# Kernel optimization log

Measured on AMD Instinct MI355X. Metric: run time of the kernel, lower is better.

Reference implementation:

```python
import jax, jax.numpy as jnp
import numpy as np

N = 10000
E = 160000
D = 512
EPS = 1e-5


def _lin_params(key, out_d, in_d, bias=True):
    k1, k2 = jax.random.split(key)
    s = 1.0 / np.sqrt(in_d)
    W = jax.random.uniform(k1, (out_d, in_d), jnp.float32, -s, s)
    if bias:
        b = jax.random.uniform(k2, (out_d,), jnp.float32, -s, s)
        return W, b
    return (W,)


def setup_inputs() -> dict:
    key = jax.random.key(0)
    ks = jax.random.split(key, 16)
    inp = {
        "x": jax.random.normal(ks[0], (N, D), jnp.float32),
        "edge_index": jax.random.randint(ks[1], (2, E), 0, N, jnp.int64),
    }
    ki = 2
    for l in range(3):
        Wp, bp = _lin_params(ks[ki], D, D); ki += 1
        Wl, bl = _lin_params(ks[ki], D, D); ki += 1
        (Wr,) = _lin_params(ks[ki], D, D, bias=False); ki += 1
        inp[f"Wp{l}"] = Wp; inp[f"bp{l}"] = bp
        inp[f"Wl{l}"] = Wl; inp[f"bl{l}"] = bl
        inp[f"Wr{l}"] = Wr
        if l < 2:  # ReLU+LayerNorm between convs
            inp[f"g{l}"] = jnp.ones((D,), jnp.float32)
            inp[f"be{l}"] = jnp.zeros((D,), jnp.float32)
    return inp


def _sage_conv(x, src, dst, Wp, bp, Wl, bl, Wr):
    # PyG SAGEConv with project=True: project+ReLU messages, mean-aggregate, lin_l + lin_r(root)
    h = jax.nn.relu(x @ Wp.T + bp)                      # [N, D] projected messages
    agg = jax.ops.segment_sum(h[src], dst, num_segments=N)   # gather + scatter-add
    cnt = jax.ops.segment_sum(jnp.ones((src.shape[0],), x.dtype), dst, num_segments=N)
    agg = agg / jnp.maximum(cnt, 1.0)[:, None]          # mean over incoming edges
    return agg @ Wl.T + bl + x @ Wr.T


def _relu_ln(x, g, b):
    x = jax.nn.relu(x)
    mu = jnp.mean(x, axis=-1, keepdims=True)
    var = jnp.mean(jnp.square(x - mu), axis=-1, keepdims=True)
    return (x - mu) * jax.lax.rsqrt(var + EPS) * g + b


def reference(x, edge_index,
              Wp0, bp0, Wl0, bl0, Wr0, g0, be0,
              Wp1, bp1, Wl1, bl1, Wr1, g1, be1,
              Wp2, bp2, Wl2, bl2, Wr2):
    src, dst = edge_index[0], edge_index[1]
    x = _sage_conv(x, src, dst, Wp0, bp0, Wl0, bl0, Wr0)
    x = _relu_ln(x, g0, be0)
    x = _sage_conv(x, src, dst, Wp1, bp1, Wl1, bl1, Wr1)
    x = _relu_ln(x, g1, be1)
    x = _sage_conv(x, src, dst, Wp2, bp2, Wl2, bl2, Wr2)
    return x
```

## Files before the change

### kernel.cpp

```cpp
#include <hip/hip_runtime.h>
#include <cstdint>

#define D 512
#define TM 128
#define TN 64
#define BK 32
#define CAP 64

typedef unsigned short u16;
typedef __bf16 bf16x8 __attribute__((ext_vector_type(8)));
typedef float f32x4 __attribute__((ext_vector_type(4)));

__device__ __forceinline__ float bf2f(u16 u) {
    unsigned int x = ((unsigned int)u) << 16;
    return __builtin_bit_cast(float, x);
}
__device__ __forceinline__ u16 f2bf(float f) {
    unsigned int x = __builtin_bit_cast(unsigned int, f);
    x += 0x7fffu + ((x >> 16) & 1u);
    return (u16)(x >> 16);
}

__device__ __forceinline__ void gload16(const u16* g, u16* l) {
    __builtin_amdgcn_global_load_lds(
        (const __attribute__((address_space(1))) void*)(uintptr_t)g,
        (__attribute__((address_space(3))) void*)(unsigned int)(uintptr_t)l,
        16, 0, 0);
}

__global__ void detect(const u16* __restrict__ xraw, const int* __restrict__ eraw,
                       int* __restrict__ flags)
{
    __shared__ int cf, ci;
    if (threadIdx.x == 0) { cf = 0; ci = 0; }
    __syncthreads();
    int t = threadIdx.x;
    u16 u = xraw[2 * t];
    int e = (u >> 7) & 0xFF;
    if (e >= 110 && e <= 129) atomicAdd(&cf, 1);
    if (eraw[2 * t + 1] == 0) atomicAdd(&ci, 1);
    __syncthreads();
    if (threadIdx.x == 0) {
        flags[0] = (cf >= 128) ? 1 : 0;
        flags[1] = (ci >= 128) ? 1 : 0;
    }
}

__global__ __launch_bounds__(256) void convert_x(
    const void* __restrict__ src, u16* __restrict__ out, const int* __restrict__ flags)
{
    int i = (blockIdx.x * 256 + threadIdx.x) * 8;
    if (flags[0]) {
        *(uint4*)(out + i) = *(const uint4*)((const u16*)src + i);
    } else {
        const float* f = (const float*)src + i;
        float4 a = *(const float4*)f;
        float4 b = *(const float4*)(f + 4);
        u16 r[8] = {f2bf(a.x), f2bf(a.y), f2bf(a.z), f2bf(a.w),
                    f2bf(b.x), f2bf(b.y), f2bf(b.z), f2bf(b.w)};
        *(uint4*)(out + i) = *(uint4*)r;
    }
}

struct Ptrs9  { const void* p[9];  };
struct Ptrs10 { const void* p[10]; };

__global__ __launch_bounds__(256) void convert_mat(
    Ptrs9 s, u16* __restrict__ out, const int* __restrict__ flags)
{
    int m = blockIdx.y;
    const void* src = s.p[m];
    u16* o = out + (size_t)m * D * D;
    int i = (blockIdx.x * 256 + threadIdx.x) * 8;
    if (flags[0]) {
        *(uint4*)(o + i) = *(const uint4*)((const u16*)src + i);
    } else {
        const float* f = (const float*)src + i;
        float4 a = *(const float4*)f;
        float4 b = *(const float4*)(f + 4);
        u16 r[8] = {f2bf(a.x), f2bf(a.y), f2bf(a.z), f2bf(a.w),
                    f2bf(b.x), f2bf(b.y), f2bf(b.z), f2bf(b.w)};
        *(uint4*)(o + i) = *(uint4*)r;
    }
}

__global__ __launch_bounds__(256) void convert_vec(
    Ptrs10 s, float* __restrict__ out, const int* __restrict__ flags)
{
    int b = blockIdx.x;
    const void* src = s.p[b];
#pragma unroll
    for (int j = threadIdx.x * 2; j < threadIdx.x * 2 + 2; j++) {
        float v = flags[0] ? bf2f(((const u16*)src)[j]) : ((const float*)src)[j];
        out[b * 512 + j] = v;
    }
}

__global__ __launch_bounds__(256) void convert_edges(
    const int* __restrict__ eraw, int* __restrict__ esrc, int* __restrict__ edst,
    const int* __restrict__ flags, int E, int Nn)
{
    int e = blockIdx.x * 256 + threadIdx.x;
    if (e >= E) return;
    int s, d;
    if (flags[1]) { s = eraw[2 * e]; d = eraw[2 * (E + e)]; }
    else          { s = eraw[e];     d = eraw[E + e]; }
    esrc[e] = min(max(s, 0), Nn - 1);
    edst[e] = min(max(d, 0), Nn - 1);
}

template <int NPASS, bool RELU, bool FINAL>
__global__ __launch_bounds__(256) void gemm_bt(
    const u16* __restrict__ A0, const u16* __restrict__ B0,
    const u16* __restrict__ A1, const u16* __restrict__ B1,
    const float* __restrict__ bias, void* __restrict__ Cout,
    const int* __restrict__ flags, int M)
{
    __shared__ __align__(16) u16 sA[TM * BK];
    __shared__ __align__(16) u16 sB[TN * BK];

    const int t    = threadIdx.x;
    const int m0   = blockIdx.x * TM;
    const int n0   = blockIdx.y * TN;
    const int wave = t >> 6, lane = t & 63;
    const int wm   = wave >> 1, wn = wave & 1;
    const int lrow = lane & 15, quad = lane >> 4;

    f32x4 acc[4][2];
#pragma unroll
    for (int i = 0; i < 4; i++)
#pragma unroll
        for (int j = 0; j < 2; j++)
#pragma unroll
            for (int r = 0; r < 4; r++) acc[i][j][r] = 0.f;

    const int cA    = (t & 3) * 8;
    const int rowA0 = min(m0 + (t >> 2),      M - 1);
    const int rowA1 = min(m0 + 64 + (t >> 2), M - 1);
    const int rowB  = n0 + (t >> 2);

#pragma unroll 1
    for (int p = 0; p < NPASS; p++) {
        const u16* A = p ? A1 : A0;
        const u16* B = p ? B1 : B0;
        const u16* gA0 = A + (size_t)rowA0 * D + cA;
        const u16* gA1 = A + (size_t)rowA1 * D + cA;
        const u16* gB  = B + (size_t)rowB  * D + cA;

#pragma unroll 1
        for (int k0 = 0; k0 < D; k0 += BK) {
            gload16(gA0 + k0, &sA[(size_t)t * 8]);
            gload16(gA1 + k0, &sA[(size_t)(t + 256) * 8]);
            gload16(gB  + k0, &sB[(size_t)t * 8]);
            __syncthreads();

            bf16x8 af[4], bfr[2];
#pragma unroll
            for (int mi = 0; mi < 4; mi++) {
                int r = wm * 64 + mi * 16 + lrow;
                af[mi] = *(const bf16x8*)&sA[r * BK + quad * 8];
            }
#pragma unroll
            for (int ni = 0; ni < 2; ni++) {
                int r = wn * 32 + ni * 16 + lrow;
                bfr[ni] = *(const bf16x8*)&sB[r * BK + quad * 8];
            }
#pragma unroll
            for (int mi = 0; mi < 4; mi++)
#pragma unroll
                for (int ni = 0; ni < 2; ni++)
                    acc[mi][ni] = __builtin_amdgcn_mfma_f32_16x16x32_bf16(
                        af[mi], bfr[ni], acc[mi][ni], 0, 0, 0);
            __syncthreads();
        }
    }

    const int out_bf16 = FINAL ? flags[0] : 1;
#pragma unroll
    for (int ni = 0; ni < 2; ni++) {
        int col = n0 + wn * 32 + ni * 16 + lrow;
        float bv = bias[col];
#pragma unroll
        for (int mi = 0; mi < 4; mi++) {
            int row0 = m0 + wm * 64 + mi * 16 + quad * 4;
#pragma unroll
            for (int r = 0; r < 4; r++) {
                int row = row0 + r;
                if (row < M) {
                    float v = acc[mi][ni][r] + bv;
                    if (RELU) v = fmaxf(v, 0.f);
                    if (!FINAL || out_bf16)
                        ((u16*)Cout)[(size_t)row * D + col] = f2bf(v);
                    else
                        ((float*)Cout)[(size_t)row * D + col] = v;
                }
            }
        }
    }
}

__global__ void build_bucket(const int* __restrict__ esrc, const int* __restrict__ edst,
                             int* __restrict__ cnt, u16* __restrict__ bucket, int E)
{
    int e = blockIdx.x * 256 + threadIdx.x;
    if (e < E) {
        int d = edst[e];
        int p = atomicAdd(&cnt[d], 1);
        if (p < CAP) bucket[(size_t)d * CAP + p] = (u16)esrc[e];
    }
}

__global__ __launch_bounds__(256) void aggregate(
    const u16* __restrict__ h, const int* __restrict__ cnt,
    const u16* __restrict__ bucket, u16* __restrict__ agg, int M)
{
    const int w = threadIdx.x >> 6, lane = threadIdx.x & 63;
    const int n = blockIdx.x * 4 + w;

    __shared__ u16 sidx[4][CAP];
    int deg = 0, dd = 0;
    if (n < M) {
        deg = cnt[n];
        dd  = min(deg, CAP);
        if (lane < dd) sidx[w][lane] = bucket[(size_t)n * CAP + lane];
    }
    __syncthreads();
    if (n >= M) return;

    float a[8] = {0.f, 0.f, 0.f, 0.f, 0.f, 0.f, 0.f, 0.f};
    int i = 0;
    for (; i + 2 <= dd; i += 2) {
        int s0 = sidx[w][i], s1 = sidx[w][i + 1];
        uint4 v0 = *(const uint4*)(h + (size_t)s0 * D + lane * 8);
        uint4 v1 = *(const uint4*)(h + (size_t)s1 * D + lane * 8);
        const unsigned int* u0 = (const unsigned int*)&v0;
        const unsigned int* u1 = (const unsigned int*)&v1;
#pragma unroll
        for (int j = 0; j < 4; j++) {
            a[2 * j]     += bf2f((u16)(u0[j] & 0xffffu)) + bf2f((u16)(u1[j] & 0xffffu));
            a[2 * j + 1] += bf2f((u16)(u0[j] >> 16))     + bf2f((u16)(u1[j] >> 16));
        }
    }
    if (i < dd) {
        int s0 = sidx[w][i];
        uint4 v0 = *(const uint4*)(h + (size_t)s0 * D + lane * 8);
        const unsigned int* u0 = (const unsigned int*)&v0;
#pragma unroll
        for (int j = 0; j < 4; j++) {
            a[2 * j]     += bf2f((u16)(u0[j] & 0xffffu));
            a[2 * j + 1] += bf2f((u16)(u0[j] >> 16));
        }
    }

    float inv = 1.f / fmaxf((float)deg, 1.f);
    u16 r[8];
#pragma unroll
    for (int j = 0; j < 8; j++) r[j] = f2bf(a[j] * inv);
    *(uint4*)(agg + (size_t)n * D + lane * 8) = *(uint4*)r;
}

__global__ __launch_bounds__(256) void relu_ln(
    const u16* __restrict__ y, const float* __restrict__ g, const float* __restrict__ be,
    u16* __restrict__ out, int M)
{
    const int row  = blockIdx.x * 4 + (threadIdx.x >> 6);
    const int lane = threadIdx.x & 63;
    if (row >= M) return;

    typedef short s16x8 __attribute__((ext_vector_type(8)));
    s16x8 v = *(const s16x8*)(y + (size_t)row * D + lane * 8);
    float f[8], s = 0.f, s2 = 0.f;
#pragma unroll
    for (int i = 0; i < 8; i++) {
        float x = bf2f((u16)v[i]);
        x = fmaxf(x, 0.f);
        f[i] = x; s += x; s2 += x * x;
    }
#pragma unroll
    for (int off = 32; off >= 1; off >>= 1) {
        s  += __shfl_xor(s, off);
        s2 += __shfl_xor(s2, off);
    }
    float mean = s * (1.f / 512.f);
    float var  = s2 * (1.f / 512.f) - mean * mean;
    float rstd = rsqrtf(var + 1e-5f);

    s16x8 res;
#pragma unroll
    for (int i = 0; i < 8; i++) {
        float o = (f[i] - mean) * rstd * g[lane * 8 + i] + be[lane * 8 + i];
        res[i] = (short)f2bf(o);
    }
    *(s16x8*)(out + (size_t)row * D + lane * 8) = res;
}

extern "C" void kernel_launch(void* const* d_in, const int* in_sizes, int n_in,
                              void* d_out, int out_size, void* d_ws, size_t ws_size,
                              hipStream_t stream)
{
    const int M = in_sizes[0] / D;
    const int E = in_sizes[1] / 2;
    const void* xraw = d_in[0];
    const int*  eraw = (const int*)d_in[1];

    const void *Wp[3], *bp[3], *Wl[3], *bl[3], *Wr[3], *g[2], *be[2];
    int idx = 2;
    for (int l = 0; l < 3; l++) {
        Wp[l] = d_in[idx++]; bp[l] = d_in[idx++];
        Wl[l] = d_in[idx++]; bl[l] = d_in[idx++];
        Wr[l] = d_in[idx++];
        if (l < 2) { g[l] = d_in[idx++]; be[l] = d_in[idx++]; }
    }

    char* w = (char*)d_ws;
    auto alloc = [&](size_t bytes) { void* p = w; w += (bytes + 255) & ~(size_t)255; return p; };
    u16*   xb     = (u16*)  alloc((size_t)M * D * 2);
    u16*   h      = (u16*)  alloc((size_t)M * D * 2);
    u16*   agg    = (u16*)  alloc((size_t)M * D * 2);
    u16*   Wb     = (u16*)  alloc((size_t)9 * D * D * 2);
    float* vecf   = (float*)alloc((size_t)10 * 512 * 4);
    int*   esrc   = (int*)  alloc((size_t)E * 4);
    int*   edst   = (int*)  alloc((size_t)E * 4);
    int*   cnt    = (int*)  alloc((size_t)M * 4);
    u16*   bucket = (u16*)  alloc((size_t)M * CAP * 2);
    int*   flags  = (int*)  alloc(256);

    detect<<<1, 256, 0, stream>>>((const u16*)xraw, eraw, flags);

    convert_x<<<dim3(M * D / (256 * 8)), dim3(256), 0, stream>>>(xraw, xb, flags);

    Ptrs9 mats;
    const void* morder[9] = {Wp[0], Wl[0], Wr[0], Wp[1], Wl[1], Wr[1], Wp[2], Wl[2], Wr[2]};
    for (int i = 0; i < 9; i++) mats.p[i] = morder[i];
    convert_mat<<<dim3(D * D / (256 * 8), 9), dim3(256), 0, stream>>>(mats, Wb, flags);

    Ptrs10 vecs;
    const void* vorder[10] = {bp[0], bl[0], g[0], be[0], bp[1], bl[1], g[1], be[1], bp[2], bl[2]};
    for (int i = 0; i < 10; i++) vecs.p[i] = vorder[i];
    convert_vec<<<dim3(10), dim3(256), 0, stream>>>(vecs, vecf, flags);

    convert_edges<<<dim3((E + 255) / 256), dim3(256), 0, stream>>>(eraw, esrc, edst, flags, E, M);

    hipMemsetAsync(cnt, 0, (size_t)M * 4, stream);
    build_bucket<<<dim3((E + 255) / 256), dim3(256), 0, stream>>>(esrc, edst, cnt, bucket, E);

    const u16* WM[9]; for (int i = 0; i < 9; i++) WM[i] = Wb + (size_t)i * D * D;
    const float* VB[10]; for (int i = 0; i < 10; i++) VB[i] = vecf + (size_t)i * 512;

    u16* yb = (u16*)d_out;
    dim3 gg((M + TM - 1) / TM, D / TN);
    const u16* xin = xb;
    for (int l = 0; l < 3; l++) {
        gemm_bt<1, true, false><<<gg, dim3(256), 0, stream>>>(
            xin, WM[l * 3 + 0], xin, WM[l * 3 + 0], VB[l * 4 + 0], h, flags, M);
        aggregate<<<dim3((M + 3) / 4), dim3(256), 0, stream>>>(h, cnt, bucket, agg, M);
        if (l < 2) {
            gemm_bt<2, false, false><<<gg, dim3(256), 0, stream>>>(
                agg, WM[l * 3 + 1], xin, WM[l * 3 + 2], VB[l * 4 + 1], yb, flags, M);
            relu_ln<<<dim3((M + 3) / 4), dim3(256), 0, stream>>>(
                yb, VB[l * 4 + 2], VB[l * 4 + 3], xb, M);
            xin = xb;
        } else {
            gemm_bt<2, false, true><<<gg, dim3(256), 0, stream>>>(
                agg, WM[l * 3 + 1], xin, WM[l * 3 + 2], VB[l * 4 + 1], d_out, flags, M);
        }
    }
}
```

Before: 368.6 us.

## Widen GEMM tile to 128x128, fuse prep kernels, unroll aggregation by four

```diff
diff --git a/kernel.cpp b/kernel.cpp
--- a/kernel.cpp
+++ b/kernel.cpp
@@ -3,7 +3,7 @@
 
 #define D 512
 #define TM 128
-#define TN 64
+#define TN 128
 #define BK 32
 #define CAP 64
 
@@ -28,29 +28,25 @@
         16, 0, 0);
 }
 
-__global__ void detect(const u16* __restrict__ xraw, const int* __restrict__ eraw,
-                       int* __restrict__ flags)
-{
-    __shared__ int cf, ci;
-    if (threadIdx.x == 0) { cf = 0; ci = 0; }
-    __syncthreads();
-    int t = threadIdx.x;
-    u16 u = xraw[2 * t];
+__device__ __forceinline__ bool is_bf16(const u16* xraw) {
+    int lane = threadIdx.x & 63;
+    u16 u = xraw[2 * lane];
     int e = (u >> 7) & 0xFF;
-    if (e >= 110 && e <= 129) atomicAdd(&cf, 1);
-    if (eraw[2 * t + 1] == 0) atomicAdd(&ci, 1);
-    __syncthreads();
-    if (threadIdx.x == 0) {
-        flags[0] = (cf >= 128) ? 1 : 0;
-        flags[1] = (ci >= 128) ? 1 : 0;
-    }
+    unsigned long long b = __ballot(e >= 110 && e <= 129);
+    return __popcll(b) >= 32;
+}
+__device__ __forceinline__ bool is_i64(const int* eraw) {
+    int lane = threadIdx.x & 63;
+    unsigned long long b = __ballot(eraw[2 * lane + 1] == 0);
+    return __popcll(b) >= 32;
 }
 
 __global__ __launch_bounds__(256) void convert_x(
-    const void* __restrict__ src, u16* __restrict__ out, const int* __restrict__ flags)
-{
+    const void* __restrict__ src, u16* __restrict__ out)
+{
+    bool bf = is_bf16((const u16*)src);
     int i = (blockIdx.x * 256 + threadIdx.x) * 8;
-    if (flags[0]) {
+    if (bf) {
         *(uint4*)(out + i) = *(const uint4*)((const u16*)src + i);
     } else {
         const float* f = (const float*)src + i;
@@ -65,48 +61,52 @@
 struct Ptrs9  { const void* p[9];  };
 struct Ptrs10 { const void* p[10]; };
 
-__global__ __launch_bounds__(256) void convert_mat(
-    Ptrs9 s, u16* __restrict__ out, const int* __restrict__ flags)
-{
+__global__ __launch_bounds__(256) void convert_wb(
+    Ptrs9 s, Ptrs10 v, u16* __restrict__ wout, float* __restrict__ vout,
+    const u16* __restrict__ xraw)
+{
+    bool bf = is_bf16(xraw);
     int m = blockIdx.y;
-    const void* src = s.p[m];
-    u16* o = out + (size_t)m * D * D;
-    int i = (blockIdx.x * 256 + threadIdx.x) * 8;
-    if (flags[0]) {
-        *(uint4*)(o + i) = *(const uint4*)((const u16*)src + i);
-    } else {
-        const float* f = (const float*)src + i;
-        float4 a = *(const float4*)f;
-        float4 b = *(const float4*)(f + 4);
-        u16 r[8] = {f2bf(a.x), f2bf(a.y), f2bf(a.z), f2bf(a.w),
-                    f2bf(b.x), f2bf(b.y), f2bf(b.z), f2bf(b.w)};
-        *(uint4*)(o + i) = *(uint4*)r;
-    }
-}
-
-__global__ __launch_bounds__(256) void convert_vec(
-    Ptrs10 s, float* __restrict__ out, const int* __restrict__ flags)
-{
-    int b = blockIdx.x;
-    const void* src = s.p[b];
-#pragma unroll
-    for (int j = threadIdx.x * 2; j < threadIdx.x * 2 + 2; j++) {
-        float v = flags[0] ? bf2f(((const u16*)src)[j]) : ((const float*)src)[j];
-        out[b * 512 + j] = v;
-    }
-}
-
-__global__ __launch_bounds__(256) void convert_edges(
-    const int* __restrict__ eraw, int* __restrict__ esrc, int* __restrict__ edst,
-    const int* __restrict__ flags, int E, int Nn)
-{
+    if (m < 9) {
+        const void* src = s.p[m];
+        u16* o = wout + (size_t)m * D * D;
+        int i = (blockIdx.x * 256 + threadIdx.x) * 8;
+        if (bf) {
+            *(uint4*)(o + i) = *(const uint4*)((const u16*)src + i);
+        } else {
+            const float* f = (const float*)src + i;
+            float4 a = *(const float4*)f;
+            float4 b = *(const float4*)(f + 4);
+            u16 r[8] = {f2bf(a.x), f2bf(a.y), f2bf(a.z), f2bf(a.w),
+                        f2bf(b.x), f2bf(b.y), f2bf(b.z), f2bf(b.w)};
+            *(uint4*)(o + i) = *(uint4*)r;
+        }
+    } else if (blockIdx.x == 0) {
+        for (int b = 0; b < 10; b++) {
+            const void* src = v.p[b];
+            for (int j = threadIdx.x * 2; j < threadIdx.x * 2 + 2; j++) {
+                float val = bf ? bf2f(((const u16*)src)[j]) : ((const float*)src)[j];
+                vout[b * 512 + j] = val;
+            }
+        }
+    }
+}
+
+__global__ void build_bucket(const int* __restrict__ eraw,
+                             int* __restrict__ cnt, u16* __restrict__ bucket,
+                             int E, int Nn)
+{
+    bool i64 = is_i64(eraw);
     int e = blockIdx.x * 256 + threadIdx.x;
-    if (e >= E) return;
-    int s, d;
-    if (flags[1]) { s = eraw[2 * e]; d = eraw[2 * (E + e)]; }
-    else          { s = eraw[e];     d = eraw[E + e]; }
-    esrc[e] = min(max(s, 0), Nn - 1);
-    edst[e] = min(max(d, 0), Nn - 1);
+    if (e < E) {
+        int s, d;
+        if (i64) { s = eraw[2 * e]; d = eraw[2 * (E + e)]; }
+        else     { s = eraw[e];     d = eraw[E + e]; }
+        s = min(max(s, 0), Nn - 1);
+        d = min(max(d, 0), Nn - 1);
+        int p = atomicAdd(&cnt[d], 1);
+        if (p < CAP) bucket[(size_t)d * CAP + p] = (u16)s;
+    }
 }
 
 template <int NPASS, bool RELU, bool FINAL>
@@ -114,7 +114,7 @@
     const u16* __restrict__ A0, const u16* __restrict__ B0,
     const u16* __restrict__ A1, const u16* __restrict__ B1,
     const float* __restrict__ bias, void* __restrict__ Cout,
-    const int* __restrict__ flags, int M)
+    const u16* __restrict__ xraw, int M)
 {
     __shared__ __align__(16) u16 sA[TM * BK];
     __shared__ __align__(16) u16 sB[TN * BK];
@@ -126,59 +126,59 @@
     const int wm   = wave >> 1, wn = wave & 1;
     const int lrow = lane & 15, quad = lane >> 4;
 
-    f32x4 acc[4][2];
+    const bool out_bf16 = FINAL ? is_bf16(xraw) : true;
+
+    f32x4 acc[4][4];
 #pragma unroll
     for (int i = 0; i < 4; i++)
 #pragma unroll
-        for (int j = 0; j < 2; j++)
+        for (int j = 0; j < 4; j++)
 #pragma unroll
             for (int r = 0; r < 4; r++) acc[i][j][r] = 0.f;
 
-    const int cA    = (t & 3) * 8;
-    const int rowA0 = min(m0 + (t >> 2),      M - 1);
-    const int rowA1 = min(m0 + 64 + (t >> 2), M - 1);
-    const int rowB  = n0 + (t >> 2);
+    const int cA  = (t & 3) * 8;
+    const int rA0 = min(m0 + (t >> 2),      M - 1);
+    const int rA1 = min(m0 + 64 + (t >> 2), M - 1);
+    const int rB0 = n0 + (t >> 2);
+    const int rB1 = n0 + 64 + (t >> 2);
 
 #pragma unroll 1
     for (int p = 0; p < NPASS; p++) {
         const u16* A = p ? A1 : A0;
         const u16* B = p ? B1 : B0;
-        const u16* gA0 = A + (size_t)rowA0 * D + cA;
-        const u16* gA1 = A + (size_t)rowA1 * D + cA;
-        const u16* gB  = B + (size_t)rowB  * D + cA;
+        const u16* gA0 = A + (size_t)rA0 * D + cA;
+        const u16* gA1 = A + (size_t)rA1 * D + cA;
+        const u16* gB0 = B + (size_t)rB0 * D + cA;
+        const u16* gB1 = B + (size_t)rB1 * D + cA;
 
 #pragma unroll 1
         for (int k0 = 0; k0 < D; k0 += BK) {
             gload16(gA0 + k0, &sA[(size_t)t * 8]);
             gload16(gA1 + k0, &sA[(size_t)(t + 256) * 8]);
-            gload16(gB  + k0, &sB[(size_t)t * 8]);
+            gload16(gB0 + k0, &sB[(size_t)t * 8]);
+            gload16(gB1 + k0, &sB[(size_t)(t + 256) * 8]);
             __syncthreads();
 
-            bf16x8 af[4], bfr[2];
-#pragma unroll
-            for (int mi = 0; mi < 4; mi++) {
-                int r = wm * 64 + mi * 16 + lrow;
-                af[mi] = *(const bf16x8*)&sA[r * BK + quad * 8];
-            }
-#pragma unroll
-            for (int ni = 0; ni < 2; ni++) {
-                int r = wn * 32 + ni * 16 + lrow;
-                bfr[ni] = *(const bf16x8*)&sB[r * BK + quad * 8];
-            }
+            bf16x8 af[4], bfr[4];
 #pragma unroll
             for (int mi = 0; mi < 4; mi++)
-#pragma unroll
-                for (int ni = 0; ni < 2; ni++)
+                af[mi] = *(const bf16x8*)&sA[(wm * 64 + mi * 16 + lrow) * BK + quad * 8];
+#pragma unroll
+            for (int ni = 0; ni < 4; ni++)
+                bfr[ni] = *(const bf16x8*)&sB[(wn * 64 + ni * 16 + lrow) * BK + quad * 8];
+#pragma unroll
+            for (int mi = 0; mi < 4; mi++)
+#pragma unroll
+                for (int ni = 0; ni < 4; ni++)
                     acc[mi][ni] = __builtin_amdgcn_mfma_f32_16x16x32_bf16(
                         af[mi], bfr[ni], acc[mi][ni], 0, 0, 0);
             __syncthreads();
         }
     }
 
-    const int out_bf16 = FINAL ? flags[0] : 1;
-#pragma unroll
-    for (int ni = 0; ni < 2; ni++) {
-        int col = n0 + wn * 32 + ni * 16 + lrow;
+#pragma unroll
+    for (int ni = 0; ni < 4; ni++) {
+        int col = n0 + wn * 64 + ni * 16 + lrow;
         float bv = bias[col];
 #pragma unroll
         for (int mi = 0; mi < 4; mi++) {
@@ -199,17 +199,6 @@
     }
 }
 
-__global__ void build_bucket(const int* __restrict__ esrc, const int* __restrict__ edst,
-                             int* __restrict__ cnt, u16* __restrict__ bucket, int E)
-{
-    int e = blockIdx.x * 256 + threadIdx.x;
-    if (e < E) {
-        int d = edst[e];
-        int p = atomicAdd(&cnt[d], 1);
-        if (p < CAP) bucket[(size_t)d * CAP + p] = (u16)esrc[e];
-    }
-}
-
 __global__ __launch_bounds__(256) void aggregate(
     const u16* __restrict__ h, const int* __restrict__ cnt,
     const u16* __restrict__ bucket, u16* __restrict__ agg, int M)
@@ -229,21 +218,25 @@
 
     float a[8] = {0.f, 0.f, 0.f, 0.f, 0.f, 0.f, 0.f, 0.f};
     int i = 0;
-    for (; i + 2 <= dd; i += 2) {
-        int s0 = sidx[w][i], s1 = sidx[w][i + 1];
-        uint4 v0 = *(const uint4*)(h + (size_t)s0 * D + lane * 8);
-        uint4 v1 = *(const uint4*)(h + (size_t)s1 * D + lane * 8);
+    for (; i + 4 <= dd; i += 4) {
+        uint4 v0 = *(const uint4*)(h + (size_t)sidx[w][i]     * D + lane * 8);
+        uint4 v1 = *(const uint4*)(h + (size_t)sidx[w][i + 1] * D + lane * 8);
+        uint4 v2 = *(const uint4*)(h + (size_t)sidx[w][i + 2] * D + lane * 8);
+        uint4 v3 = *(const uint4*)(h + (size_t)sidx[w][i + 3] * D + lane * 8);
         const unsigned int* u0 = (const unsigned int*)&v0;
         const unsigned int* u1 = (const unsigned int*)&v1;
+        const unsigned int* u2 = (const unsigned int*)&v2;
+        const unsigned int* u3 = (const unsigned int*)&v3;
 #pragma unroll
         for (int j = 0; j < 4; j++) {
-            a[2 * j]     += bf2f((u16)(u0[j] & 0xffffu)) + bf2f((u16)(u1[j] & 0xffffu));
-            a[2 * j + 1] += bf2f((u16)(u0[j] >> 16))     + bf2f((u16)(u1[j] >> 16));
-        }
-    }
-    if (i < dd) {
-        int s0 = sidx[w][i];
-        uint4 v0 = *(const uint4*)(h + (size_t)s0 * D + lane * 8);
+            a[2 * j]     += bf2f((u16)(u0[j] & 0xffffu)) + bf2f((u16)(u1[j] & 0xffffu))
+                          + bf2f((u16)(u2[j] & 0xffffu)) + bf2f((u16)(u3[j] & 0xffffu));
+            a[2 * j + 1] += bf2f((u16)(u0[j] >> 16)) + bf2f((u16)(u1[j] >> 16))
+                          + bf2f((u16)(u2[j] >> 16)) + bf2f((u16)(u3[j] >> 16));
+        }
+    }
+    for (; i < dd; i++) {
+        uint4 v0 = *(const uint4*)(h + (size_t)sidx[w][i] * D + lane * 8);
         const unsigned int* u0 = (const unsigned int*)&v0;
 #pragma unroll
         for (int j = 0; j < 4; j++) {
@@ -319,30 +312,22 @@
     u16*   agg    = (u16*)  alloc((size_t)M * D * 2);
     u16*   Wb     = (u16*)  alloc((size_t)9 * D * D * 2);
     float* vecf   = (float*)alloc((size_t)10 * 512 * 4);
-    int*   esrc   = (int*)  alloc((size_t)E * 4);
-    int*   edst   = (int*)  alloc((size_t)E * 4);
     int*   cnt    = (int*)  alloc((size_t)M * 4);
     u16*   bucket = (u16*)  alloc((size_t)M * CAP * 2);
-    int*   flags  = (int*)  alloc(256);
-
-    detect<<<1, 256, 0, stream>>>((const u16*)xraw, eraw, flags);
-
-    convert_x<<<dim3(M * D / (256 * 8)), dim3(256), 0, stream>>>(xraw, xb, flags);
+
+    convert_x<<<dim3(M * D / (256 * 8)), dim3(256), 0, stream>>>(xraw, xb);
 
     Ptrs9 mats;
     const void* morder[9] = {Wp[0], Wl[0], Wr[0], Wp[1], Wl[1], Wr[1], Wp[2], Wl[2], Wr[2]};
     for (int i = 0; i < 9; i++) mats.p[i] = morder[i];
-    convert_mat<<<dim3(D * D / (256 * 8), 9), dim3(256), 0, stream>>>(mats, Wb, flags);
-
     Ptrs10 vecs;
     const void* vorder[10] = {bp[0], bl[0], g[0], be[0], bp[1], bl[1], g[1], be[1], bp[2], bl[2]};
     for (int i = 0; i < 10; i++) vecs.p[i] = vorder[i];
-    convert_vec<<<dim3(10), dim3(256), 0, stream>>>(vecs, vecf, flags);
-
-    convert_edges<<<dim3((E + 255) / 256), dim3(256), 0, stream>>>(eraw, esrc, edst, flags, E, M);
+    convert_wb<<<dim3(D * D / (256 * 8), 10), dim3(256), 0, stream>>>(
+        mats, vecs, Wb, vecf, (const u16*)xraw);
 
     hipMemsetAsync(cnt, 0, (size_t)M * 4, stream);
-    build_bucket<<<dim3((E + 255) / 256), dim3(256), 0, stream>>>(esrc, edst, cnt, bucket, E);
+    build_bucket<<<dim3((E + 255) / 256), dim3(256), 0, stream>>>(eraw, cnt, bucket, E, M);
 
     const u16* WM[9]; for (int i = 0; i < 9; i++) WM[i] = Wb + (size_t)i * D * D;
     const float* VB[10]; for (int i = 0; i < 10; i++) VB[i] = vecf + (size_t)i * 512;
@@ -352,17 +337,17 @@
     const u16* xin = xb;
     for (int l = 0; l < 3; l++) {
         gemm_bt<1, true, false><<<gg, dim3(256), 0, stream>>>(
-            xin, WM[l * 3 + 0], xin, WM[l * 3 + 0], VB[l * 4 + 0], h, flags, M);
+            xin, WM[l * 3 + 0], xin, WM[l * 3 + 0], VB[l * 4 + 0], h, (const u16*)xraw, M);
         aggregate<<<dim3((M + 3) / 4), dim3(256), 0, stream>>>(h, cnt, bucket, agg, M);
         if (l < 2) {
             gemm_bt<2, false, false><<<gg, dim3(256), 0, stream>>>(
-                agg, WM[l * 3 + 1], xin, WM[l * 3 + 2], VB[l * 4 + 1], yb, flags, M);
+                agg, WM[l * 3 + 1], xin, WM[l * 3 + 2], VB[l * 4 + 1], yb, (const u16*)xraw, M);
             relu_ln<<<dim3((M + 3) / 4), dim3(256), 0, stream>>>(
                 yb, VB[l * 4 + 2], VB[l * 4 + 3], xb, M);
             xin = xb;
         } else {
             gemm_bt<2, false, true><<<gg, dim3(256), 0, stream>>>(
-                agg, WM[l * 3 + 1], xin, WM[l * 3 + 2], VB[l * 4 + 1], d_out, flags, M);
-        }
-    }
-}
+                agg, WM[l * 3 + 1], xin, WM[l * 3 + 2], VB[l * 4 + 1], d_out, (const u16*)xraw, M);
+        }
+    }
+}
```

New measurement: 381.0 us. +3.3%, slower.
